# Optimization experiments

Hardware: AMD Instinct MI355X
Metric: run time of the kernel (lower is better)

The kernel has to match this reference:

```python
import jax, jax.numpy as jnp
import numpy as np

N_NODES = 100000
N_EDGES = 1600000
IN_CH = 128
DIM = 128
OUT_CH = 10
NUM_GRAPHS = 128
BN_EPS = 1e-5


def _bn_train(h, gamma, beta):
    # BatchNorm1d in training mode: batch statistics over the node axis
    mean = jnp.mean(h, axis=0)
    var = jnp.var(h, axis=0)
    return (h - mean) * jax.lax.rsqrt(var + BN_EPS) * gamma + beta


def _gin_conv(x, src, dst, W1, b1, gamma, beta, W2, b2):
    # GINConv with eps=0: nn(x + sum_{j in N(i)} x_j)
    agg = jax.ops.segment_sum(x[src], dst, num_segments=x.shape[0])  # [N, d]
    h = (x + agg) @ W1 + b1
    h = jax.nn.relu(_bn_train(h, gamma, beta))
    h = jax.nn.relu(h @ W2 + b2)
    return h


def setup_inputs() -> dict:
    key = jax.random.key(0)
    ks = jax.random.split(key, 16)
    s = 0.02
    inp = {
        "x": jax.random.normal(ks[0], (N_NODES, IN_CH), dtype=jnp.float32),
        "edge_index": jax.random.randint(ks[1], (2, N_EDGES), 0, N_NODES, dtype=jnp.int64),
        "batch": jnp.sort(jax.random.randint(ks[2], (N_NODES,), 0, NUM_GRAPHS, dtype=jnp.int64)),
        # conv1 MLP
        "W1a": jax.random.normal(ks[3], (IN_CH, DIM), dtype=jnp.float32) * s,
        "b1a": jnp.zeros((DIM,), jnp.float32),
        "ga": jnp.ones((DIM,), jnp.float32),
        "ba": jnp.zeros((DIM,), jnp.float32),
        "W2a": jax.random.normal(ks[4], (DIM, DIM), dtype=jnp.float32) * s,
        "b2a": jnp.zeros((DIM,), jnp.float32),
        # conv2 MLP
        "W1b": jax.random.normal(ks[5], (DIM, DIM), dtype=jnp.float32) * s,
        "b1b": jnp.zeros((DIM,), jnp.float32),
        "gb": jnp.ones((DIM,), jnp.float32),
        "bb": jnp.zeros((DIM,), jnp.float32),
        "W2b": jax.random.normal(ks[6], (DIM, DIM), dtype=jnp.float32) * s,
        "b2b": jnp.zeros((DIM,), jnp.float32),
        # readout linears
        "Wl1": jax.random.normal(ks[7], (DIM, DIM), dtype=jnp.float32) * s,
        "bl1": jnp.zeros((DIM,), jnp.float32),
        "Wl2": jax.random.normal(ks[8], (DIM, OUT_CH), dtype=jnp.float32) * s,
        "bl2": jnp.zeros((OUT_CH,), jnp.float32),
    }
    return inp


def reference(x, edge_index, batch, W1a, b1a, ga, ba, W2a, b2a,
              W1b, b1b, gb, bb, W2b, b2b, Wl1, bl1, Wl2, bl2):
    src, dst = edge_index[0], edge_index[1]
    h = _gin_conv(x, src, dst, W1a, b1a, ga, ba, W2a, b2a)
    h = _gin_conv(h, src, dst, W1b, b1b, gb, bb, W2b, b2b)
    pooled = jax.ops.segment_sum(h, batch, num_segments=NUM_GRAPHS)  # [G, d]
    out = jax.nn.relu(pooled @ Wl1 + bl1)
    # dropout p=0.5 is identity in deterministic/eval evaluation
    out = out @ Wl2 + bl2
    return out
```

## Files before the change

kernel.cpp:

```cpp
#include <hip/hip_runtime.h>

#define N_NODES    100000
#define N_EDGES    1600000
#define DIM        128
#define OUT_CH     10
#define NUM_GRAPHS 128
#define BN_EPS     1e-5f

#define BSHIFT   8
#define NB2      391
#define CAP2     5120
#define NTILES   782
#define GEMM_GRID 256

typedef __attribute__((ext_vector_type(8))) short short8;
typedef __attribute__((ext_vector_type(4))) float floatx4;

__device__ inline float bf2f(unsigned short u) {
    union { unsigned i; float f; } v; v.i = (unsigned)u << 16; return v.f;
}
__device__ inline unsigned short f2bf(float f) {
    union { float f; unsigned i; } v; v.f = f;
    return (unsigned short)((v.i + 0x8000u) >> 16);
}

__device__ inline void async_cp16(const unsigned short* g, unsigned short* l) {
    __builtin_amdgcn_global_load_lds(
        (const __attribute__((address_space(1))) void*)g,
        (__attribute__((address_space(3))) void*)l, 16, 0, 0);
}

__global__ void k_cvt_x(const float* __restrict__ x, unsigned short* __restrict__ xb,
                        int* __restrict__ gcur, float* __restrict__ stats4,
                        float* __restrict__ pooled) {
    int t = threadIdx.x;
    if (blockIdx.x == 0) {
        for (int i = t; i < NB2 + 1; i += 256) gcur[i] = 0;
        for (int i = t; i < 4 * DIM; i += 256) stats4[i] = 0.f;
        for (int i = t; i < NUM_GRAPHS * DIM; i += 256) pooled[i] = 0.f;
    }
    int idx = blockIdx.x * 256 + t;
    float4 v = ((const float4*)x)[idx];
    ushort4 o;
    o.x = f2bf(v.x); o.y = f2bf(v.y); o.z = f2bf(v.z); o.w = f2bf(v.w);
    ((ushort4*)xb)[idx] = o;
}

__global__ void k_prep_w(const float* __restrict__ W0, const float* __restrict__ W1,
                         const float* __restrict__ W2, const float* __restrict__ W3,
                         unsigned short* __restrict__ Wt) {
    const float* Ws[4] = {W0, W1, W2, W3};
    const float* W = Ws[blockIdx.y];
    unsigned short* o = Wt + blockIdx.y * (DIM * DIM);
    int idx = blockIdx.x * 256 + threadIdx.x;
    int n = idx >> 7, k = idx & 127;
    o[idx] = f2bf(W[k * DIM + n]);
}

__global__ __launch_bounds__(256)
void k_bucket(const int* __restrict__ src, const int* __restrict__ dst,
              int* __restrict__ gcur, unsigned* __restrict__ pairs) {
    __shared__ int cnt[NB2 + 1];
    __shared__ int lofs[NB2 + 1];
    __shared__ int gbase[NB2 + 1];
    __shared__ int scanA[256], scanB[256];
    __shared__ int stage[8192];

    int t = threadIdx.x;
    for (int i = t; i < NB2 + 1; i += 256) cnt[i] = 0;
    __syncthreads();
    int base = blockIdx.x * 8192;
    int n_e = min(8192, N_EDGES - base);
    for (int i = t; i < n_e; i += 256)
        atomicAdd(&cnt[dst[base + i] >> BSHIFT], 1);
    __syncthreads();
    int vA = cnt[t];
    int vB = (t < NB2 - 256) ? cnt[256 + t] : 0;
    scanA[t] = vA; scanB[t] = vB;
    __syncthreads();
    for (int off = 1; off < 256; off <<= 1) {
        int tA = (t >= off) ? scanA[t - off] : 0;
        int tB = (t >= off) ? scanB[t - off] : 0;
        __syncthreads();
        scanA[t] += tA; scanB[t] += tB;
        __syncthreads();
    }
    lofs[t] = scanA[t] - vA;
    if (t < NB2 - 256) lofs[256 + t] = scanA[255] + scanB[t] - vB;
    __syncthreads();
    for (int i = t; i < NB2; i += 256) {
        gbase[i] = (cnt[i] > 0) ? atomicAdd(&gcur[i], cnt[i]) : 0;
        cnt[i] = lofs[i];
    }
    __syncthreads();
    for (int i = t; i < n_e; i += 256) {
        int d = dst[base + i];
        int b = d >> BSHIFT;
        int pos = atomicAdd(&cnt[b], 1);
        stage[pos] = (int)(((unsigned)src[base + i] << 8) | (unsigned)(d & 255));
    }
    __syncthreads();
    int w = t >> 6, lane = t & 63;
    for (int b = w; b < NB2; b += 4) {
        int len = cnt[b] - lofs[b];
        int g0  = gbase[b];
        int maxlen = CAP2 - g0; if (maxlen < 0) maxlen = 0;
        if (len > maxlen) len = maxlen;
        unsigned* dp = pairs + (size_t)b * CAP2 + g0;
        const int* sp = stage + lofs[b];
        for (int i = lane; i < len; i += 64) dp[i] = (unsigned)sp[i];
    }
}

__global__ void k_bscan(const int* __restrict__ gcur, int* __restrict__ bbase,
                        int* __restrict__ row_ptr) {
    __shared__ int sh[512];
    int t = threadIdx.x;
    int v = (t < NB2) ? min(gcur[t], CAP2) : 0;
    sh[t] = v; __syncthreads();
    for (int off = 1; off < 512; off <<= 1) {
        int tmp = (t >= off) ? sh[t - off] : 0;
        __syncthreads();
        sh[t] += tmp;
        __syncthreads();
    }
    if (t < NB2) bbase[t] = sh[t] - v;
    if (t == NB2 - 1) { bbase[NB2] = sh[t]; row_ptr[N_NODES] = sh[t]; }
}

__global__ __launch_bounds__(256)
void k_csr(const unsigned* __restrict__ pairs, const int* __restrict__ gcur,
           const int* __restrict__ bbase, int* __restrict__ row_ptr,
           int* __restrict__ col) {
    __shared__ int hist[256];
    __shared__ int cur[256];
    __shared__ int stage[CAP2];
    int bi = blockIdx.x, t = threadIdx.x;
    hist[t] = 0; __syncthreads();
    int n = min(gcur[bi], CAP2);
    const unsigned* P = pairs + (size_t)bi * CAP2;
    for (int i = t; i < n; i += 256)
        atomicAdd(&hist[P[i] & 255u], 1);
    __syncthreads();
    int self = hist[t];
    cur[t] = self; __syncthreads();
    for (int off = 1; off < 256; off <<= 1) {
        int tmp = (t >= off) ? cur[t - off] : 0;
        __syncthreads();
        cur[t] += tmp;
        __syncthreads();
    }
    int excl = cur[t] - self;
    int base = bbase[bi];
    int node = (bi << 8) + t;
    if (node < N_NODES) row_ptr[node] = base + excl;
    cur[t] = excl;
    __syncthreads();
    for (int i = t; i < n; i += 256) {
        unsigned e = P[i];
        int pos = atomicAdd(&cur[e & 255u], 1);
        stage[pos] = (int)(e >> 8);
    }
    __syncthreads();
    for (int i = t; i < n; i += 256) col[base + i] = stage[i];
}

__global__ void k_agg(const unsigned short* __restrict__ X,
                      unsigned short* __restrict__ Out,
                      const int* __restrict__ row_ptr, const int* __restrict__ col) {
    int wid = (blockIdx.x * 256 + threadIdx.x) >> 6;
    if (wid >= N_NODES) return;
    int lane = threadIdx.x & 63;
    int half = lane >> 5, m = lane & 31;
    const ushort4* X4 = (const ushort4*)X;

    float a0=0.f,a1=0.f,a2=0.f,a3=0.f;
    float c0=0.f,c1=0.f,c2=0.f,c3=0.f;
    if (half == 0) {
        ushort4 sv = X4[(size_t)wid * 32 + m];
        a0 = bf2f(sv.x); a1 = bf2f(sv.y); a2 = bf2f(sv.z); a3 = bf2f(sv.w);
    }
    int s = row_ptr[wid], e = row_ptr[wid + 1];
    int p = s + half;
    for (; p + 6 < e; p += 8) {
        int v0i = col[p], v1i = col[p + 2], v2i = col[p + 4], v3i = col[p + 6];
        ushort4 v0 = X4[(size_t)v0i * 32 + m];
        ushort4 v1 = X4[(size_t)v1i * 32 + m];
        ushort4 v2 = X4[(size_t)v2i * 32 + m];
        ushort4 v3 = X4[(size_t)v3i * 32 + m];
        a0 += bf2f(v0.x); a1 += bf2f(v0.y); a2 += bf2f(v0.z); a3 += bf2f(v0.w);
        c0 += bf2f(v1.x); c1 += bf2f(v1.y); c2 += bf2f(v1.z); c3 += bf2f(v1.w);
        a0 += bf2f(v2.x); a1 += bf2f(v2.y); a2 += bf2f(v2.z); a3 += bf2f(v2.w);
        c0 += bf2f(v3.x); c1 += bf2f(v3.y); c2 += bf2f(v3.z); c3 += bf2f(v3.w);
    }
    for (; p < e; p += 2) {
        ushort4 v = X4[(size_t)col[p] * 32 + m];
        a0 += bf2f(v.x); a1 += bf2f(v.y); a2 += bf2f(v.z); a3 += bf2f(v.w);
    }
    a0 += c0; a1 += c1; a2 += c2; a3 += c3;
    a0 += __shfl_xor(a0, 32);
    a1 += __shfl_xor(a1, 32);
    a2 += __shfl_xor(a2, 32);
    a3 += __shfl_xor(a3, 32);
    if (half == 0) {
        ushort4 o;
        o.x = f2bf(a0); o.y = f2bf(a1); o.z = f2bf(a2); o.w = f2bf(a3);
        ((ushort4*)Out)[(size_t)wid * 32 + m] = o;
    }
}

template<bool BN_LOAD, bool STATS, bool RELU_ST>
__global__ __launch_bounds__(256)
void k_gemm(const unsigned short* __restrict__ In, unsigned short* __restrict__ Out,
            const unsigned short* __restrict__ Wt, const float* __restrict__ bias,
            const float* __restrict__ ssum_in, const float* __restrict__ ssq_in,
            const float* __restrict__ gamma, const float* __restrict__ beta,
            float* __restrict__ ssum_out, float* __restrict__ ssq_out) {
    __shared__ __align__(16) unsigned short sB[128 * 128];
    __shared__ float ssc[128], ssh[128];
    __shared__ float s_sum[128], s_sq[128];

    int t = threadIdx.x;
    int w = t >> 6, lane = t & 63;
    int m = lane & 15;
    int q = lane >> 4;
    int sw = m & 7;

    #pragma unroll
    for (int u = 0; u < 8; ++u) {
        int i = (w * 8 + u) * 64 + lane;
        int n = i >> 4, p = i & 15;
        async_cp16(Wt + n * 128 + ((p ^ (n & 7)) << 3), sB + (size_t)(w * 8 + u) * 512);
    }
    if (BN_LOAD && t < 128) {
        float mn  = ssum_in[t] * (1.0f / N_NODES);
        float var = ssq_in[t] * (1.0f / N_NODES) - mn * mn;
        float inv = rsqrtf(var + BN_EPS);
        float sc  = gamma[t] * inv;
        ssc[t] = sc; ssh[t] = beta[t] - mn * sc;
    }
    if (STATS && t < 128) { s_sum[t] = 0.f; s_sq[t] = 0.f; }

    int tile = blockIdx.x;
    short8 a0[4], a1[4];
    {
        int rA0 = min(tile * 128 + w * 32 + m,      N_NODES - 1);
        int rA1 = min(tile * 128 + w * 32 + 16 + m, N_NODES - 1);
        #pragma unroll
        for (int kk = 0; kk < 4; ++kk) {
            a0[kk] = *(const short8*)(In + (size_t)rA0 * 128 + kk * 32 + q * 8);
            a1[kk] = *(const short8*)(In + (size_t)rA1 * 128 + kk * 32 + q * 8);
        }
    }
    __syncthreads();

    #pragma unroll 1
    for (; tile < NTILES; ) {
        int next = tile + GEMM_GRID;
        short8 b0[4], b1[4];
        if (next < NTILES) {
            int rN0 = min(next * 128 + w * 32 + m,      N_NODES - 1);
            int rN1 = min(next * 128 + w * 32 + 16 + m, N_NODES - 1);
            #pragma unroll
            for (int kk = 0; kk < 4; ++kk) {
                b0[kk] = *(const short8*)(In + (size_t)rN0 * 128 + kk * 32 + q * 8);
                b1[kk] = *(const short8*)(In + (size_t)rN1 * 128 + kk * 32 + q * 8);
            }
        }

        if (BN_LOAD) {
            #pragma unroll
            for (int kk = 0; kk < 4; ++kk) {
                int base = kk * 32 + q * 8;
                #pragma unroll
                for (int j = 0; j < 8; ++j) {
                    float scj = ssc[base + j], shj = ssh[base + j];
                    float f0 = fmaxf(bf2f((unsigned short)a0[kk][j]) * scj + shj, 0.f);
                    float f1 = fmaxf(bf2f((unsigned short)a1[kk][j]) * scj + shj, 0.f);
                    a0[kk][j] = (short)f2bf(f0);
                    a1[kk][j] = (short)f2bf(f1);
                }
            }
        }

        floatx4 acc[2][8] = {};
        #pragma unroll
        for (int kk = 0; kk < 4; ++kk) {
            int cp = (kk * 4 + q) ^ sw;
            #pragma unroll
            for (int c = 0; c < 8; ++c) {
                int nr = c * 16 + m;
                short8 b = *(const short8*)&sB[nr * 128 + (cp << 3)];
                acc[0][c] = __builtin_amdgcn_mfma_f32_16x16x32_bf16(b, a0[kk], acc[0][c], 0, 0, 0);
                acc[1][c] = __builtin_amdgcn_mfma_f32_16x16x32_bf16(b, a1[kk], acc[1][c], 0, 0, 0);
            }
        }

        int r0 = tile * 128;
        #pragma unroll
        for (int c = 0; c < 8; ++c) {
            int ch0 = c * 16 + q * 4;
            float4 bv = *(const float4*)(bias + ch0);
            float sr[4] = {0,0,0,0}, qr[4] = {0,0,0,0};
            #pragma unroll
            for (int h = 0; h < 2; ++h) {
                int node = r0 + w * 32 + h * 16 + m;
                float v0 = acc[h][c][0] + bv.x;
                float v1 = acc[h][c][1] + bv.y;
                float v2 = acc[h][c][2] + bv.z;
                float v3 = acc[h][c][3] + bv.w;
                if (RELU_ST) {
                    v0 = fmaxf(v0, 0.f); v1 = fmaxf(v1, 0.f);
                    v2 = fmaxf(v2, 0.f); v3 = fmaxf(v3, 0.f);
                }
                if (node < N_NODES) {
                    ushort4 o;
                    o.x = f2bf(v0); o.y = f2bf(v1); o.z = f2bf(v2); o.w = f2bf(v3);
                    *(ushort4*)(Out + (size_t)node * 128 + ch0) = o;
                    if (STATS) {
                        sr[0] += v0; sr[1] += v1; sr[2] += v2; sr[3] += v3;
                        qr[0] += v0*v0; qr[1] += v1*v1; qr[2] += v2*v2; qr[3] += v3*v3;
                    }
                }
            }
            if (STATS) {
                #pragma unroll
                for (int msk = 1; msk <= 8; msk <<= 1) {
                    #pragma unroll
                    for (int r = 0; r < 4; ++r) {
                        sr[r] += __shfl_xor(sr[r], msk);
                        qr[r] += __shfl_xor(qr[r], msk);
                    }
                }
                if (m == 0) {
                    #pragma unroll
                    for (int r = 0; r < 4; ++r) {
                        atomicAdd(&s_sum[ch0 + r], sr[r]);
                        atomicAdd(&s_sq [ch0 + r], qr[r]);
                    }
                }
            }
        }

        tile = next;
        if (tile < NTILES) {
            #pragma unroll
            for (int kk = 0; kk < 4; ++kk) { a0[kk] = b0[kk]; a1[kk] = b1[kk]; }
        }
    }

    if (STATS) {
        __syncthreads();
        if (t < 128) {
            atomicAdd(&ssum_out[t], s_sum[t]);
            atomicAdd(&ssq_out [t], s_sq[t]);
        }
    }
}

#define POOL_BLOCKS 782
#define POOL_CHUNK  128
__global__ __launch_bounds__(256)
void k_pool(const unsigned short* __restrict__ h, const int* __restrict__ batch,
            float* __restrict__ pooled) {
    int t  = threadIdx.x;
    int cq = (t & 31) * 4;
    int r  = t >> 5;
    int n0 = blockIdx.x * POOL_CHUNK;
    if (n0 >= N_NODES) return;
    int n1 = min(n0 + POOL_CHUNK, N_NODES);
    float a0=0.f, a1=0.f, a2=0.f, a3=0.f;
    int g = -1;
    for (int i = n0 + r; i < n1; i += 8) {
        int gi = batch[i];
        if (gi != g) {
            if (g >= 0) {
                atomicAdd(&pooled[g * DIM + cq + 0], a0);
                atomicAdd(&pooled[g * DIM + cq + 1], a1);
                atomicAdd(&pooled[g * DIM + cq + 2], a2);
                atomicAdd(&pooled[g * DIM + cq + 3], a3);
            }
            a0 = a1 = a2 = a3 = 0.f; g = gi;
        }
        ushort4 v = *(const ushort4*)(h + (size_t)i * DIM + cq);
        a0 += bf2f(v.x); a1 += bf2f(v.y); a2 += bf2f(v.z); a3 += bf2f(v.w);
    }
    if (g >= 0) {
        atomicAdd(&pooled[g * DIM + cq + 0], a0);
        atomicAdd(&pooled[g * DIM + cq + 1], a1);
        atomicAdd(&pooled[g * DIM + cq + 2], a2);
        atomicAdd(&pooled[g * DIM + cq + 3], a3);
    }
}

__global__ void k_readout(const float* __restrict__ pooled,
                          const float* __restrict__ Wl1, const float* __restrict__ bl1,
                          const float* __restrict__ Wl2, const float* __restrict__ bl2,
                          float* __restrict__ out) {
    __shared__ float p[128], r[128];
    int g = blockIdx.x, c = threadIdx.x;
    p[c] = pooled[g * DIM + c];
    __syncthreads();
    float s = bl1[c];
    #pragma unroll 8
    for (int k = 0; k < DIM; ++k) s += p[k] * Wl1[k * DIM + c];
    r[c] = fmaxf(s, 0.f);
    __syncthreads();
    if (c < OUT_CH) {
        float s2 = bl2[c];
        #pragma unroll 8
        for (int k = 0; k < DIM; ++k) s2 += r[k] * Wl2[k * OUT_CH + c];
        out[g * OUT_CH + c] = s2;
    }
}

extern "C" void kernel_launch(void* const* d_in, const int* in_sizes, int n_in,
                              void* d_out, int out_size, void* d_ws, size_t ws_size,
                              hipStream_t stream) {
    const float* x   = (const float*)d_in[0];
    const int*   ei  = (const int*)d_in[1];
    const int*   bat = (const int*)d_in[2];
    const float* W1a = (const float*)d_in[3];
    const float* b1a = (const float*)d_in[4];
    const float* ga  = (const float*)d_in[5];
    const float* ba  = (const float*)d_in[6];
    const float* W2a = (const float*)d_in[7];
    const float* b2a = (const float*)d_in[8];
    const float* W1b = (const float*)d_in[9];
    const float* b1b = (const float*)d_in[10];
    const float* gb  = (const float*)d_in[11];
    const float* bbt = (const float*)d_in[12];
    const float* W2b = (const float*)d_in[13];
    const float* b2b = (const float*)d_in[14];
    const float* Wl1 = (const float*)d_in[15];
    const float* bl1 = (const float*)d_in[16];
    const float* Wl2 = (const float*)d_in[17];
    const float* bl2 = (const float*)d_in[18];
    float* out = (float*)d_out;

    const int* src = ei;
    const int* dst = ei + N_EDGES;

    char* w = (char*)d_ws;
    size_t off = 0;
    auto alloc = [&](size_t bytes) -> char* {
        char* p = w + off; off += (bytes + 255) & ~(size_t)255; return p;
    };
    unsigned short* xb   = (unsigned short*)alloc((size_t)N_NODES * DIM * 2);
    unsigned short* nb0  = (unsigned short*)alloc((size_t)N_NODES * DIM * 2);
    unsigned short* nb1  = (unsigned short*)alloc((size_t)N_NODES * DIM * 2);
    unsigned short* Wtb  = (unsigned short*)alloc((size_t)4 * DIM * DIM * 2);
    unsigned* pairs = (unsigned*)alloc((size_t)NB2 * CAP2 * 4);
    int*   row_ptr = (int*)  alloc((size_t)(N_NODES + 1) * 4);
    int*   col     = (int*)  alloc((size_t)N_EDGES * 4);
    int*   gcur    = (int*)  alloc((NB2 + 1) * 4);
    int*   bbase   = (int*)  alloc((NB2 + 1) * 4);
    float* stats4  = (float*)alloc((size_t)4 * DIM * 4);
    float* pooled  = (float*)alloc((size_t)NUM_GRAPHS * DIM * 4);
    float* ssumA = stats4, *ssqA = stats4 + DIM, *ssumB = stats4 + 2*DIM, *ssqB = stats4 + 3*DIM;

    k_cvt_x<<<(N_NODES * DIM / 4) / 256, 256, 0, stream>>>(x, xb, gcur, stats4, pooled);
    k_prep_w<<<dim3(64, 4), 256, 0, stream>>>(W1a, W2a, W1b, W2b, Wtb);
    const unsigned short* Wt1a = Wtb;
    const unsigned short* Wt2a = Wtb + DIM * DIM;
    const unsigned short* Wt1b = Wtb + 2 * DIM * DIM;
    const unsigned short* Wt2b = Wtb + 3 * DIM * DIM;

    k_bucket<<<(N_EDGES + 8191) / 8192, 256, 0, stream>>>(src, dst, gcur, pairs);
    k_bscan<<<1, 512, 0, stream>>>(gcur, bbase, row_ptr);
    k_csr<<<NB2, 256, 0, stream>>>(pairs, gcur, bbase, row_ptr, col);

    int agg_blocks = (N_NODES * 64) / 256;

    k_agg<<<agg_blocks, 256, 0, stream>>>(xb, nb0, row_ptr, col);
    k_gemm<false, true, false><<<GEMM_GRID, 256, 0, stream>>>(
        nb0, nb1, Wt1a, b1a, nullptr, nullptr, nullptr, nullptr, ssumA, ssqA);
    k_gemm<true, false, true><<<GEMM_GRID, 256, 0, stream>>>(
        nb1, nb0, Wt2a, b2a, ssumA, ssqA, ga, ba, nullptr, nullptr);
    k_agg<<<agg_blocks, 256, 0, stream>>>(nb0, nb1, row_ptr, col);
    k_gemm<false, true, false><<<GEMM_GRID, 256, 0, stream>>>(
        nb1, nb0, Wt1b, b1b, nullptr, nullptr, nullptr, nullptr, ssumB, ssqB);
    k_gemm<true, false, true><<<GEMM_GRID, 256, 0, stream>>>(
        nb0, nb1, Wt2b, b2b, ssumB, ssqB, gb, bbt, nullptr, nullptr);
    k_pool<<<POOL_BLOCKS, 256, 0, stream>>>(nb1, bat, pooled);
    k_readout<<<NUM_GRAPHS, 128, 0, stream>>>(pooled, Wl1, bl1, Wl2, bl2, out);
}
```

Measured before the change: 451.3 us.

## Shard aggregation by feature slices across XCDs for L2-resident gathers

Rewrites the neighbor aggregation so each of 8 block groups (selected by blockIdx mod 8) gathers only a 32-byte slice of every node's feature row, with 16 edges processed in parallel per wave and a grid-stride loop over nodes. The intent is that each shard's slice of the feature matrix fits in a single XCD's L2, turning random gathers into cache hits. In exchange the CSR index arrays are read eight times and each gather is a small 32-byte access; nontemporal loads/stores are used for indices and output.

```diff
diff --git a/kernel.cpp b/kernel.cpp
--- a/kernel.cpp
+++ b/kernel.cpp
@@ -12,6 +12,8 @@
 #define CAP2     5120
 #define NTILES   782
 #define GEMM_GRID 256
+
+#define AGG_SHARD_GROUPS 2048
 
 typedef __attribute__((ext_vector_type(8))) short short8;
 typedef __attribute__((ext_vector_type(4))) float floatx4;
@@ -165,47 +167,47 @@
     for (int i = t; i < n; i += 256) col[base + i] = stage[i];
 }
 
-__global__ void k_agg(const unsigned short* __restrict__ X,
-                      unsigned short* __restrict__ Out,
-                      const int* __restrict__ row_ptr, const int* __restrict__ col) {
-    int wid = (blockIdx.x * 256 + threadIdx.x) >> 6;
-    if (wid >= N_NODES) return;
-    int lane = threadIdx.x & 63;
-    int half = lane >> 5, m = lane & 31;
+__global__ __launch_bounds__(256)
+void k_agg(const unsigned short* __restrict__ X,
+           unsigned short* __restrict__ Out,
+           const int* __restrict__ row_ptr, const int* __restrict__ col) {
+    int t = threadIdx.x;
+    int w = t >> 6, lane = t & 63;
+    int c = lane & 3;
+    int e = lane >> 2;
+    int shard = blockIdx.x & 7;
+    int cb = (shard << 2) + c;
     const ushort4* X4 = (const ushort4*)X;
-
-    float a0=0.f,a1=0.f,a2=0.f,a3=0.f;
-    float c0=0.f,c1=0.f,c2=0.f,c3=0.f;
-    if (half == 0) {
-        ushort4 sv = X4[(size_t)wid * 32 + m];
-        a0 = bf2f(sv.x); a1 = bf2f(sv.y); a2 = bf2f(sv.z); a3 = bf2f(sv.w);
-    }
-    int s = row_ptr[wid], e = row_ptr[wid + 1];
-    int p = s + half;
-    for (; p + 6 < e; p += 8) {
-        int v0i = col[p], v1i = col[p + 2], v2i = col[p + 4], v3i = col[p + 6];
-        ushort4 v0 = X4[(size_t)v0i * 32 + m];
-        ushort4 v1 = X4[(size_t)v1i * 32 + m];
-        ushort4 v2 = X4[(size_t)v2i * 32 + m];
-        ushort4 v3 = X4[(size_t)v3i * 32 + m];
-        a0 += bf2f(v0.x); a1 += bf2f(v0.y); a2 += bf2f(v0.z); a3 += bf2f(v0.w);
-        c0 += bf2f(v1.x); c1 += bf2f(v1.y); c2 += bf2f(v1.z); c3 += bf2f(v1.w);
-        a0 += bf2f(v2.x); a1 += bf2f(v2.y); a2 += bf2f(v2.z); a3 += bf2f(v2.w);
-        c0 += bf2f(v3.x); c1 += bf2f(v3.y); c2 += bf2f(v3.z); c3 += bf2f(v3.w);
-    }
-    for (; p < e; p += 2) {
-        ushort4 v = X4[(size_t)col[p] * 32 + m];
-        a0 += bf2f(v.x); a1 += bf2f(v.y); a2 += bf2f(v.z); a3 += bf2f(v.w);
-    }
-    a0 += c0; a1 += c1; a2 += c2; a3 += c3;
-    a0 += __shfl_xor(a0, 32);
-    a1 += __shfl_xor(a1, 32);
-    a2 += __shfl_xor(a2, 32);
-    a3 += __shfl_xor(a3, 32);
-    if (half == 0) {
-        ushort4 o;
-        o.x = f2bf(a0); o.y = f2bf(a1); o.z = f2bf(a2); o.w = f2bf(a3);
-        ((ushort4*)Out)[(size_t)wid * 32 + m] = o;
+    int G = gridDim.x >> 3;
+
+    for (int g = blockIdx.x >> 3; g < (N_NODES + 3) / 4; g += G) {
+        int n = g * 4 + w;
+        if (n >= N_NODES) continue;
+        int s  = __builtin_nontemporal_load(&row_ptr[n]);
+        int en = __builtin_nontemporal_load(&row_ptr[n + 1]);
+        float a0 = 0.f, a1 = 0.f, a2 = 0.f, a3 = 0.f;
+        for (int p = s + e; p < en; p += 16) {
+            int v = __builtin_nontemporal_load(&col[p]);
+            ushort4 xv = X4[(size_t)v * 32 + cb];
+            a0 += bf2f(xv.x); a1 += bf2f(xv.y); a2 += bf2f(xv.z); a3 += bf2f(xv.w);
+        }
+        #pragma unroll
+        for (int msk = 4; msk <= 32; msk <<= 1) {
+            a0 += __shfl_xor(a0, msk);
+            a1 += __shfl_xor(a1, msk);
+            a2 += __shfl_xor(a2, msk);
+            a3 += __shfl_xor(a3, msk);
+        }
+        if (e == 0) {
+            ushort4 sv = X4[(size_t)n * 32 + cb];
+            a0 += bf2f(sv.x); a1 += bf2f(sv.y); a2 += bf2f(sv.z); a3 += bf2f(sv.w);
+            unsigned long long pk =
+                  (unsigned long long)f2bf(a0)
+                | ((unsigned long long)f2bf(a1) << 16)
+                | ((unsigned long long)f2bf(a2) << 32)
+                | ((unsigned long long)f2bf(a3) << 48);
+            __builtin_nontemporal_store(pk, (unsigned long long*)Out + (size_t)n * 32 + cb);
+        }
     }
 }
 
@@ -470,14 +472,14 @@
     k_bscan<<<1, 512, 0, stream>>>(gcur, bbase, row_ptr);
     k_csr<<<NB2, 256, 0, stream>>>(pairs, gcur, bbase, row_ptr, col);
 
-    int agg_blocks = (N_NODES * 64) / 256;
-
-    k_agg<<<agg_blocks, 256, 0, stream>>>(xb, nb0, row_ptr, col);
+    int agg_grid = 8 * AGG_SHARD_GROUPS;
+
+    k_agg<<<agg_grid, 256, 0, stream>>>(xb, nb0, row_ptr, col);
     k_gemm<false, true, false><<<GEMM_GRID, 256, 0, stream>>>(
         nb0, nb1, Wt1a, b1a, nullptr, nullptr, nullptr, nullptr, ssumA, ssqA);
     k_gemm<true, false, true><<<GEMM_GRID, 256, 0, stream>>>(
         nb1, nb0, Wt2a, b2a, ssumA, ssqA, ga, ba, nullptr, nullptr);
-    k_agg<<<agg_blocks, 256, 0, stream>>>(nb0, nb1, row_ptr, col);
+    k_agg<<<agg_grid, 256, 0, stream>>>(nb0, nb1, row_ptr, col);
     k_gemm<false, true, false><<<GEMM_GRID, 256, 0, stream>>>(
         nb1, nb0, Wt1b, b1b, nullptr, nullptr, nullptr, nullptr, ssumB, ssqB);
     k_gemm<true, false, true><<<GEMM_GRID, 256, 0, stream>>>(
```

Measured after the change: 911.2 us. 2.02x slower.
